# Optimization experiments

Hardware: AMD Instinct MI355X
Metric: run time of the kernel (lower is better)

The kernel has to match this reference:

```python
import jax, jax.numpy as jnp
import numpy as np

# Matches init_kwargs: zip(dilation_rates, sequence_lengths)
DILATION_RATES = (1, 2, 4)
SEQUENCE_LENGTHS = (2048, 4096, 8192)


def setup_inputs() -> dict:
    key = jax.random.key(0)
    qkv = jax.random.normal(key, (4, 8192, 3, 16, 64), dtype=jnp.float32)
    return {"qkv": qkv}


def _attend(x, scale):
    # x: (B', Nseg, 3, h, d) -- vanilla softmax attention over axis Nseg
    q, k, v = x[:, :, 0], x[:, :, 1], x[:, :, 2]
    scores = jnp.einsum('bnhd,bmhd->bhnm', q, k) * scale
    attn = jax.nn.softmax(scores, axis=-1)
    return jnp.einsum('bhnm,bmhd->bnhd', attn, v)  # (B', Nseg, h, d)


def reference(qkv):
    b, n, _, h, d = qkv.shape
    scale = 1.0 / jnp.sqrt(jnp.asarray(d, qkv.dtype))  # softmax_scale=None default
    out = jnp.zeros((b, n, h, d), qkv.dtype)
    for r, s in zip(DILATION_RATES, SEQUENCE_LENGTHS):
        nseg = n // s
        # 'b (n s) qkv h d -> b n s qkv h d' then dilated slice [::r]
        x = qkv.reshape(b, nseg, s, 3, h, d)[:, :, ::r]  # (b, nseg, sp, 3, h, d)
        sp = x.shape[2]
        # 'b n s qkv h d -> (b s) n qkv h d'
        x = x.transpose(0, 2, 1, 3, 4, 5).reshape(b * sp, nseg, 3, h, d)
        o = _attend(x, scale)  # (b*sp, nseg, h, d)
        # '(b s) n h d -> b n s h d'
        o = o.reshape(b, sp, nseg, h, d).transpose(0, 2, 1, 3, 4)
        # strided scatter-add back into the full-length accumulator
        out = out.reshape(b, nseg, s, h, d).at[:, :, ::r].add(o).reshape(b, n, h, d)
    # final global normalization over the sequence dim (as in the source)
    return out / out.sum(axis=1, keepdims=True)
```

## Files before the change

### kernel.cpp

```cpp
#include <hip/hip_runtime.h>

constexpr int   Bn    = 4;
constexpr int   Nn    = 8192;
constexpr int   Hn    = 16;
constexpr int   Dn    = 64;
constexpr int   ROW   = 3 * Hn * Dn;
constexpr long long QKV_B = (long long)Nn * ROW;
constexpr int   OUT_N = Hn * Dn;
constexpr long long OUT_B = (long long)Nn * OUT_N;
constexpr long long OUT_TOT = (long long)Bn * OUT_B;
constexpr int   NBLK  = 2048;
constexpr int   BLKS_PER_B = 512;

using v4f = __attribute__((ext_vector_type(4))) float;
using v4u = __attribute__((ext_vector_type(4))) unsigned int;

template<int CTRL>
__device__ __forceinline__ float dpp_add(float x) {
  int mv = __builtin_amdgcn_update_dpp(0, __float_as_int(x), CTRL, 0xF, 0xF, true);
  return x + __int_as_float(mv);
}
__device__ __forceinline__ float row16_sum(float x) {
  x = dpp_add<0xB1>(x);
  x = dpp_add<0x4E>(x);
  x = dpp_add<0x124>(x);
  x = dpp_add<0x128>(x);
  return x;
}

__device__ __forceinline__ unsigned short f2bf_rne(float x) {
  unsigned u = __float_as_uint(x);
  u += 0x7FFFu + ((u >> 16) & 1u);
  return (unsigned short)(u >> 16);
}

struct Frag {
  float q[4][4], k[4][4], v[4][4];
};

__device__ __forceinline__ void load_frag(Frag& f, const float* __restrict__ qb,
                                          int j) {
#pragma unroll
  for (int m = 0; m < 4; ++m) {
    const float* rp = qb + (size_t)(m * 2048 + j) * ROW;
    float4 t;
    t = *(const float4*)(rp);
    f.q[m][0] = t.x; f.q[m][1] = t.y; f.q[m][2] = t.z; f.q[m][3] = t.w;
    t = *(const float4*)(rp + 1024);
    f.k[m][0] = t.x; f.k[m][1] = t.y; f.k[m][2] = t.z; f.k[m][3] = t.w;
    t = *(const float4*)(rp + 2048);
    f.v[m][0] = t.x; f.v[m][1] = t.y; f.v[m][2] = t.z; f.v[m][3] = t.w;
  }
}

template<bool USE_BF16>
__device__ __forceinline__ void compute_frag(const Frag& f, int j, size_t obase,
                                             float* __restrict__ out,
                                             unsigned short* __restrict__ ws16,
                                             float* cs) {
  float S[4][4];
#pragma unroll
  for (int m = 0; m < 4; ++m)
#pragma unroll
    for (int m2 = 0; m2 < 4; ++m2) {
      float s = f.q[m][0] * f.k[m2][0] + f.q[m][1] * f.k[m2][1] +
                f.q[m][2] * f.k[m2][2] + f.q[m][3] * f.k[m2][3];
      S[m][m2] = row16_sum(s) * 0.125f;
    }

  float acc[4][4];

#pragma unroll
  for (int m = 0; m < 4; ++m) {
    float mx = fmaxf(fmaxf(S[m][0], S[m][1]), fmaxf(S[m][2], S[m][3]));
    float e0 = __expf(S[m][0] - mx);
    float e1 = __expf(S[m][1] - mx);
    float e2 = __expf(S[m][2] - mx);
    float e3 = __expf(S[m][3] - mx);
    float inv = 1.0f / (e0 + e1 + e2 + e3);
    e0 *= inv; e1 *= inv; e2 *= inv; e3 *= inv;
#pragma unroll
    for (int c = 0; c < 4; ++c)
      acc[m][c] = e0 * f.v[0][c] + e1 * f.v[1][c] +
                  e2 * f.v[2][c] + e3 * f.v[3][c];
  }

  if ((j & 1) == 0) {
#pragma unroll
    for (int m = 0; m < 4; ++m) {
      const int a  = m & 1;
      const int b2 = a + 2;
      float sa = S[m][a], sb = S[m][b2];
      float mx = fmaxf(sa, sb);
      float ea = __expf(sa - mx);
      float eb = __expf(sb - mx);
      float inv = 1.0f / (ea + eb);
      ea *= inv; eb *= inv;
#pragma unroll
      for (int c = 0; c < 4; ++c)
        acc[m][c] += ea * f.v[a][c] + eb * f.v[b2][c];
    }
  }

  if ((j & 3) == 0) {
#pragma unroll
    for (int m = 0; m < 4; ++m)
#pragma unroll
      for (int c = 0; c < 4; ++c)
        acc[m][c] += f.v[m][c];
  }

#pragma unroll
  for (int m = 0; m < 4; ++m) {
    const size_t oi = obase + (size_t)(m * 2048 + j) * OUT_N;
    if (USE_BF16) {
      ushort4 st;
      st.x = f2bf_rne(acc[m][0]); st.y = f2bf_rne(acc[m][1]);
      st.z = f2bf_rne(acc[m][2]); st.w = f2bf_rne(acc[m][3]);
      *(ushort4*)(ws16 + oi) = st;
    } else {
      *(float4*)(out + oi) =
          make_float4(acc[m][0], acc[m][1], acc[m][2], acc[m][3]);
    }
    cs[0] += acc[m][0]; cs[1] += acc[m][1];
    cs[2] += acc[m][2]; cs[3] += acc[m][3];
  }
}

template<bool USE_BF16>
__global__ __launch_bounds__(256) void dil_main(const float* __restrict__ qkv,
                                                float* __restrict__ out,
                                                unsigned short* __restrict__ ws16,
                                                float* __restrict__ partial) {
  const int tid  = threadIdx.x;
  const int bid  = blockIdx.x;
  const int b    = bid >> 9;
  const int j0   = (bid & 511) * 4;

  const float* qb = qkv + (size_t)b * QKV_B + tid * 4;
  const size_t obase = (size_t)b * OUT_B + tid * 4;

  float cs[4] = {0.f, 0.f, 0.f, 0.f};

  Frag A, B;
  load_frag(A, qb, j0);
  load_frag(B, qb, j0 + 1);
  compute_frag<USE_BF16>(A, j0, obase, out, ws16, cs);
  load_frag(A, qb, j0 + 2);
  compute_frag<USE_BF16>(B, j0 + 1, obase, out, ws16, cs);
  load_frag(B, qb, j0 + 3);
  compute_frag<USE_BF16>(A, j0 + 2, obase, out, ws16, cs);
  compute_frag<USE_BF16>(B, j0 + 3, obase, out, ws16, cs);

  *(float4*)(partial + (size_t)bid * 1024 + tid * 4) =
      make_float4(cs[0], cs[1], cs[2], cs[3]);
}

__global__ __launch_bounds__(256) void dil_recip(const float* __restrict__ partial,
                                                 float* __restrict__ recip) {
  const int i = blockIdx.x * 256 + threadIdx.x;
  const int b = i >> 10;
  const int w = i & 1023;
  const float* p = partial + (size_t)b * BLKS_PER_B * 1024 + w;
  double s = 0.0;
  for (int r = 0; r < BLKS_PER_B; ++r)
    s += (double)p[(size_t)r * 1024];
  recip[i] = (float)(1.0 / s);
}

__global__ __launch_bounds__(256) void dil_scale_bf16(const unsigned short* __restrict__ ws16,
                                                      float* __restrict__ out,
                                                      const float* __restrict__ recip) {
  const long long u = (long long)blockIdx.x * 256 + threadIdx.x;
  const long long e = u * 8;
  const int b  = (int)(e >> 23);
  const int h  = (int)((e >> 6) & 15);
  const int q8 = (int)((e >> 3) & 7);

  const float4 r0 = ((const float4*)recip)[((b * 16 + h) << 4) + q8 * 2];
  const float4 r1 = ((const float4*)recip)[((b * 16 + h) << 4) + q8 * 2 + 1];

  const v4u raw = __builtin_nontemporal_load((const v4u*)(ws16 + e));
  v4f o0, o1;
  o0[0] = __uint_as_float((raw[0] & 0xFFFFu) << 16) * r0.x;
  o0[1] = __uint_as_float((raw[0] & 0xFFFF0000u))   * r0.y;
  o0[2] = __uint_as_float((raw[1] & 0xFFFFu) << 16) * r0.z;
  o0[3] = __uint_as_float((raw[1] & 0xFFFF0000u))   * r0.w;
  o1[0] = __uint_as_float((raw[2] & 0xFFFFu) << 16) * r1.x;
  o1[1] = __uint_as_float((raw[2] & 0xFFFF0000u))   * r1.y;
  o1[2] = __uint_as_float((raw[3] & 0xFFFFu) << 16) * r1.z;
  o1[3] = __uint_as_float((raw[3] & 0xFFFF0000u))   * r1.w;
  __builtin_nontemporal_store(o0, (v4f*)(out + e));
  __builtin_nontemporal_store(o1, (v4f*)(out + e + 4));
}

__global__ __launch_bounds__(256) void dil_scale_f32(float* __restrict__ out,
                                                     const float* __restrict__ recip) {
  const long long f = (long long)blockIdx.x * 256 + threadIdx.x;
  const int d4 = (int)(f & 15);
  const int h  = (int)((f >> 4) & 15);
  const int b  = (int)(f >> 21);
  const float4 r = ((const float4*)recip)[(b * 16 + h) * 16 + d4];
  float4 o = ((const float4*)out)[f];
  o.x *= r.x; o.y *= r.y; o.z *= r.z; o.w *= r.w;
  ((float4*)out)[f] = o;
}

extern "C" void kernel_launch(void* const* d_in, const int* in_sizes, int n_in,
                              void* d_out, int out_size, void* d_ws, size_t ws_size,
                              hipStream_t stream) {
  const float* qkv = (const float*)d_in[0];
  float* out = (float*)d_out;

  const size_t bf16_bytes    = (size_t)OUT_TOT * 2;
  const size_t partial_bytes = (size_t)NBLK * 1024 * 4;
  const size_t recip_bytes   = 4096 * sizeof(float);

  bool use_bf16 = (bf16_bytes + partial_bytes + recip_bytes) <= ws_size;

  unsigned short* ws16 = (unsigned short*)d_ws;
  char* tail = (char*)d_ws + (use_bf16 ? bf16_bytes : 0);
  float* partial = (float*)tail;
  float* recip   = (float*)(tail + partial_bytes);

  if (use_bf16)
    dil_main<true><<<NBLK, 256, 0, stream>>>(qkv, out, ws16, partial);
  else
    dil_main<false><<<NBLK, 256, 0, stream>>>(qkv, out, ws16, partial);

  dil_recip<<<16, 256, 0, stream>>>(partial, recip);

  if (use_bf16) {
    const long long nu = OUT_TOT / 8;
    dil_scale_bf16<<<(int)(nu / 256), 256, 0, stream>>>(ws16, out, recip);
  } else {
    const long long nf4 = OUT_TOT / 4;
    dil_scale_f32<<<(int)(nf4 / 256), 256, 0, stream>>>(out, recip);
  }
}
```

Measured before the change: 155.8 us.

## Fuse main, reciprocal and scale kernels into one cooperative grid-sync kernel

Replaces the three-kernel sequence with a single cooperative kernel that computes attention fragments, grid-syncs, reduces column sums with wave shuffles, grid-syncs again, and rescales the bf16 workspace into the output. Each block handles multiple 8-row units, which halves the partial-sum buffer. The goal is to remove two kernel launch gaps and the serial single-thread column reduction. In exchange, grid-wide barriers and reduced grid size can lower occupancy and latency hiding, and the scale pass uses narrower per-thread accesses than the old vectorized scale kernel.

```diff
diff --git a/kernel.cpp b/kernel.cpp
--- a/kernel.cpp
+++ b/kernel.cpp
@@ -1,4 +1,7 @@
 #include <hip/hip_runtime.h>
+#include <hip/hip_cooperative_groups.h>
+
+namespace cg = cooperative_groups;
 
 constexpr int   Bn    = 4;
 constexpr int   Nn    = 8192;
@@ -11,6 +14,7 @@
 constexpr long long OUT_TOT = (long long)Bn * OUT_B;
 constexpr int   NBLK  = 2048;
 constexpr int   BLKS_PER_B = 512;
+constexpr int   UNITS = 1024;
 
 using v4f = __attribute__((ext_vector_type(4))) float;
 using v4u = __attribute__((ext_vector_type(4))) unsigned int;
@@ -32,6 +36,9 @@
   unsigned u = __float_as_uint(x);
   u += 0x7FFFu + ((u >> 16) & 1u);
   return (unsigned short)(u >> 16);
+}
+__device__ __forceinline__ float bf2f(unsigned short u) {
+  return __uint_as_float(((unsigned)u) << 16);
 }
 
 struct Frag {
@@ -124,6 +131,85 @@
     }
     cs[0] += acc[m][0]; cs[1] += acc[m][1];
     cs[2] += acc[m][2]; cs[3] += acc[m][3];
+  }
+}
+
+template<bool USE_BF16>
+__global__ __launch_bounds__(256) void dil_fused(const float* __restrict__ qkv,
+                                                 float* __restrict__ out,
+                                                 unsigned short* __restrict__ ws16,
+                                                 float* __restrict__ partial,
+                                                 float* __restrict__ recip,
+                                                 int unitsPerBlk) {
+  cg::grid_group grid = cg::this_grid();
+  const int tid = threadIdx.x;
+
+  for (int uu = 0; uu < unitsPerBlk; ++uu) {
+    const int unit = blockIdx.x * unitsPerBlk + uu;
+    const int b    = unit >> 8;
+    const int j0   = (unit & 255) * 8;
+    const float* qb = qkv + (size_t)b * QKV_B + tid * 4;
+    const size_t obase = (size_t)b * OUT_B + tid * 4;
+    float cs[4] = {0.f, 0.f, 0.f, 0.f};
+    for (int it = 0; it < 8; ++it) {
+      Frag f;
+      load_frag(f, qb, j0 + it);
+      compute_frag<USE_BF16>(f, j0 + it, obase, out, ws16, cs);
+    }
+    *(float4*)(partial + (size_t)unit * 1024 + tid * 4) =
+        make_float4(cs[0], cs[1], cs[2], cs[3]);
+  }
+
+  __threadfence();
+  grid.sync();
+
+  {
+    const int nWaves = (gridDim.x * 256) >> 6;
+    const int waveId = (blockIdx.x * 256 + tid) >> 6;
+    const int lane   = tid & 63;
+    for (int col = waveId; col < 4096; col += nWaves) {
+      const int b = col >> 10;
+      const int w = col & 1023;
+      const float* p = partial + (size_t)(b * 256) * 1024 + w;
+      double s = 0.0;
+#pragma unroll
+      for (int i = 0; i < 4; ++i)
+        s += (double)p[(size_t)(lane * 4 + i) * 1024];
+#pragma unroll
+      for (int off = 32; off; off >>= 1)
+        s += __shfl_xor(s, off, 64);
+      if (lane == 0) recip[col] = (float)(1.0 / s);
+    }
+  }
+
+  __threadfence();
+  grid.sync();
+
+  for (int uu = 0; uu < unitsPerBlk; ++uu) {
+    const int unit = blockIdx.x * unitsPerBlk + uu;
+    const int b    = unit >> 8;
+    const int j0   = (unit & 255) * 8;
+    const size_t obase = (size_t)b * OUT_B + tid * 4;
+    const float4 r = *(const float4*)(recip + b * 1024 + tid * 4);
+    for (int it = 0; it < 8; ++it) {
+      const int j = j0 + it;
+#pragma unroll
+      for (int m = 0; m < 4; ++m) {
+        const size_t oi = obase + (size_t)(m * 2048 + j) * OUT_N;
+        float4 o;
+        if (USE_BF16) {
+          const ushort4 raw = *(const ushort4*)(ws16 + oi);
+          o.x = bf2f(raw.x) * r.x;
+          o.y = bf2f(raw.y) * r.y;
+          o.z = bf2f(raw.z) * r.z;
+          o.w = bf2f(raw.w) * r.w;
+        } else {
+          o = *(const float4*)(out + oi);
+          o.x *= r.x; o.y *= r.y; o.z *= r.z; o.w *= r.w;
+        }
+        *(float4*)(out + oi) = o;
+      }
+    }
   }
 }
 
@@ -213,15 +299,44 @@
   float* out = (float*)d_out;
 
   const size_t bf16_bytes    = (size_t)OUT_TOT * 2;
-  const size_t partial_bytes = (size_t)NBLK * 1024 * 4;
+  const size_t partialF_bytes = (size_t)UNITS * 1024 * 4;
+  const size_t partialK_bytes = (size_t)NBLK * 1024 * 4;
   const size_t recip_bytes   = 4096 * sizeof(float);
 
-  bool use_bf16 = (bf16_bytes + partial_bytes + recip_bytes) <= ws_size;
-
+  int dev = 0;
+  hipGetDevice(&dev);
+  int coop = 0;
+  hipDeviceGetAttribute(&coop, hipDeviceAttributeCooperativeLaunch, dev);
+  int numCU = 0;
+  hipDeviceGetAttribute(&numCU, hipDeviceAttributeMultiprocessorCount, dev);
+  int occ = 0;
+  hipOccupancyMaxActiveBlocksPerMultiprocessor(&occ, dil_fused<true>, 256, 0);
+
+  const bool ws_ok_fused =
+      (bf16_bytes + partialF_bytes + recip_bytes) <= ws_size;
+  const int maxResident = occ * numCU;
+  int G = 0;
+  if (maxResident >= 1024) G = 1024;
+  else if (maxResident >= 512) G = 512;
+  else if (maxResident >= 256) G = 256;
+
+  if (coop && ws_ok_fused && G > 0) {
+    unsigned short* ws16 = (unsigned short*)d_ws;
+    float* partial = (float*)((char*)d_ws + bf16_bytes);
+    float* recip   = (float*)((char*)d_ws + bf16_bytes + partialF_bytes);
+    int upb = UNITS / G;
+    void* args[] = {(void*)&qkv, (void*)&out, (void*)&ws16,
+                    (void*)&partial, (void*)&recip, (void*)&upb};
+    hipLaunchCooperativeKernel(reinterpret_cast<const void*>(&dil_fused<true>),
+                               dim3(G), dim3(256), args, 0, stream);
+    return;
+  }
+
+  bool use_bf16 = (bf16_bytes + partialK_bytes + recip_bytes) <= ws_size;
   unsigned short* ws16 = (unsigned short*)d_ws;
   char* tail = (char*)d_ws + (use_bf16 ? bf16_bytes : 0);
   float* partial = (float*)tail;
-  float* recip   = (float*)(tail + partial_bytes);
+  float* recip   = (float*)(tail + partialK_bytes);
 
   if (use_bf16)
     dil_main<true><<<NBLK, 256, 0, stream>>>(qkv, out, ws16, partial);
```

After: 417.6 us. +168.1%, slower.
